# Kernel tuning notes

Measured on AMD Instinct MI355X. Metric: run time of the kernel, lower is better.

Reference implementation:

```python
import jax, jax.numpy as jnp
import numpy as np

C = 4096
N = 16384


def setup_inputs() -> dict:
    key = jax.random.key(0)
    k1, k2, k3 = jax.random.split(key, 3)
    x = jax.random.normal(k1, (N, C), dtype=jnp.float32)
    # fc params, torch default init: U(-1/sqrt(C), 1/sqrt(C))
    bound = 1.0 / np.sqrt(C)
    W = jax.random.uniform(k2, (C, C), dtype=jnp.float32, minval=-bound, maxval=bound)
    b = jax.random.uniform(k3, (C,), dtype=jnp.float32, minval=-bound, maxval=bound)
    return {"x": x, "W": W, "b": b, "scale_factor": 2}


def reference(x, W, b, scale_factor):
    # MyGAP_fc: mean over batch -> [1, C] (kept as [C])
    x_gap = jnp.mean(x, axis=0)                      # [C]
    # fc: torch Linear y = x @ W.T + b
    x_scale = x_gap @ W.T + b                        # [C]
    x_scale = jax.nn.sigmoid(x_scale * scale_factor) # [C]
    # training-mode path (no hard thresholding)
    # MyScale_fc: per-channel broadcast multiply
    x_out = x * x_scale[None, :]                     # [N, C]
    return (x_out, x_scale)
```

## Files before the change

kernel.cpp:

```cpp
#include <hip/hip_runtime.h>

#define C 4096
#define NROWS 16384
#define NBLK 256
#define TPB 1024
#define RPB 64
#define HWREG_XCC_ID 63508

typedef float f32x4 __attribute__((ext_vector_type(4)));

__device__ __forceinline__ unsigned aload(unsigned* p) {
    return __hip_atomic_load(p, __ATOMIC_RELAXED, __HIP_MEMORY_SCOPE_AGENT);
}
__device__ __forceinline__ unsigned aadd(unsigned* p, unsigned v) {
    return __hip_atomic_fetch_add(p, v, __ATOMIC_RELAXED, __HIP_MEMORY_SCOPE_AGENT);
}

#define CTRL_WORDS 2048

__device__ __forceinline__ void gbar(unsigned* ctrl, unsigned r, bool& lead,
                                     unsigned xcd) {
    __syncthreads();
    if (threadIdx.x == 0) {
        if (r == 1) {
            if (aadd(&ctrl[512 + 64 * xcd], 1u) == 0) {
                lead = true;
                unsigned lv = aadd(&ctrl[1088], 1u);
                asm volatile("" :: "v"(lv) : "memory");
            }
        }
        aadd(&ctrl[64 * xcd], 1u);
        if (lead) {
            for (;;) {
                unsigned s = 0;
#pragma unroll
                for (int i = 0; i < 8; ++i) s += aload(&ctrl[64 * i]);
                if (s >= r * NBLK) break;
                __builtin_amdgcn_s_sleep(2);
            }
            unsigned v = __hip_atomic_fetch_add(&ctrl[1024], 0u, __ATOMIC_ACQ_REL,
                                                __HIP_MEMORY_SCOPE_AGENT);
            asm volatile("" :: "v"(v) : "memory");
            aadd(&ctrl[1152], 1u);
            while (aload(&ctrl[1152]) < r * aload(&ctrl[1088]))
                __builtin_amdgcn_s_sleep(2);
            __hip_atomic_store(&ctrl[1280 + 64 * xcd], r, __ATOMIC_RELAXED,
                               __HIP_MEMORY_SCOPE_AGENT);
        } else {
            while (aload(&ctrl[1280 + 64 * xcd]) < r) __builtin_amdgcn_s_sleep(8);
        }
    }
    __syncthreads();
}

__global__ __launch_bounds__(TPB, 4)
void fused_kernel(const float* __restrict__ x, const float* __restrict__ W,
                  const float* __restrict__ b, const int* __restrict__ sf,
                  float* __restrict__ out, float* __restrict__ ws) {
    float* gsumX = ws;
    unsigned* ctrl = (unsigned*)(ws + 8 * (size_t)C);

    __shared__ float g_lds[C];

    const int t = threadIdx.x;
    const int bidx = blockIdx.x;
    const int r0 = bidx * RPB;
    const float sf0 = (float)sf[0];
    const unsigned xcd = __builtin_amdgcn_s_getreg(HWREG_XCC_ID) & 7u;
    bool lead = false;

    {
        const f32x4* xv = (const f32x4*)x + (size_t)r0 * (C / 4) + t;
        f32x4 acc = {0.f, 0.f, 0.f, 0.f};
#pragma unroll 8
        for (int r = 0; r < RPB; ++r)
            acc += xv[(size_t)r * (C / 4)];
        float* g = gsumX + (size_t)xcd * C + t * 4;
        atomicAdd(g + 0, acc.x);
        atomicAdd(g + 1, acc.y);
        atomicAdd(g + 2, acc.z);
        atomicAdd(g + 3, acc.w);
    }
    gbar(ctrl, 1, lead, xcd);

    {
        f32x4 s = {0.f, 0.f, 0.f, 0.f};
#pragma unroll
        for (int xx = 0; xx < 8; ++xx)
            s += ((const f32x4*)(gsumX + (size_t)xx * C))[t];
        ((f32x4*)g_lds)[t] = s;
    }
    __syncthreads();
    {
        const int wave = t >> 6, lane = t & 63;
        const int row = (bidx << 4) + wave;
        const f32x4* wv = (const f32x4*)(W + (size_t)row * C);
        const f32x4* gv = (const f32x4*)g_lds;
        float acc = 0.f;
#pragma unroll
        for (int i = 0; i < 16; ++i) {
            const f32x4 w4 = __builtin_nontemporal_load(wv + (i << 6) + lane);
            const f32x4 g4 = gv[(i << 6) + lane];
            acc += w4.x * g4.x + w4.y * g4.y + w4.z * g4.z + w4.w * g4.w;
        }
#pragma unroll
        for (int off = 32; off; off >>= 1) acc += __shfl_down(acc, off);
        if (lane == 0) {
            const float y = acc * (1.0f / NROWS) + b[row];
            out[(size_t)NROWS * C + row] = 1.0f / (1.0f + __expf(-sf0 * y));
        }
    }
    gbar(ctrl, 2, lead, xcd);

    {
        const f32x4 sc = ((const f32x4*)(out + (size_t)NROWS * C))[t];
        const f32x4* xv = (const f32x4*)x + (size_t)r0 * (C / 4) + t;
        f32x4* ov = (f32x4*)out + (size_t)r0 * (C / 4) + t;
#pragma unroll 8
        for (int r = 0; r < RPB; ++r) {
            f32x4 v = xv[(size_t)r * (C / 4)];
            v *= sc;
            __builtin_nontemporal_store(v, ov + (size_t)r * (C / 4));
        }
    }
}

extern "C" void kernel_launch(void* const* d_in, const int* in_sizes, int n_in,
                              void* d_out, int out_size, void* d_ws, size_t ws_size,
                              hipStream_t stream) {
    const float* x = (const float*)d_in[0];
    const float* W = (const float*)d_in[1];
    const float* b = (const float*)d_in[2];
    const int* sf  = (const int*)d_in[3];

    float* out = (float*)d_out;
    float* ws  = (float*)d_ws;

    hipMemsetAsync(d_ws, 0, (8 * (size_t)C) * sizeof(float)
                            + CTRL_WORDS * sizeof(unsigned), stream);

    fused_kernel<<<NBLK, TPB, 0, stream>>>(x, W, b, sf, out, ws);
}
```

Measured before the change: 180.7 us.

## Split column-sum into separate kernels and keep one grid barrier

```diff
diff --git a/kernel.cpp b/kernel.cpp
--- a/kernel.cpp
+++ b/kernel.cpp
@@ -2,10 +2,10 @@
 
 #define C 4096
 #define NROWS 16384
-#define NBLK 256
-#define TPB 1024
-#define RPB 64
+#define NBLK 512
 #define HWREG_XCC_ID 63508
+#define PARTS 256
+#define CTRL_WORDS 2048
 
 typedef float f32x4 __attribute__((ext_vector_type(4)));
 
@@ -16,18 +16,14 @@
     return __hip_atomic_fetch_add(p, v, __ATOMIC_RELAXED, __HIP_MEMORY_SCOPE_AGENT);
 }
 
-#define CTRL_WORDS 2048
-
-__device__ __forceinline__ void gbar(unsigned* ctrl, unsigned r, bool& lead,
-                                     unsigned xcd) {
+__device__ __forceinline__ void gbar(unsigned* ctrl, unsigned xcd) {
+    bool lead = false;
     __syncthreads();
     if (threadIdx.x == 0) {
-        if (r == 1) {
-            if (aadd(&ctrl[512 + 64 * xcd], 1u) == 0) {
-                lead = true;
-                unsigned lv = aadd(&ctrl[1088], 1u);
-                asm volatile("" :: "v"(lv) : "memory");
-            }
+        if (aadd(&ctrl[512 + 64 * xcd], 1u) == 0) {
+            lead = true;
+            unsigned lv = aadd(&ctrl[1088], 1u);
+            asm volatile("" :: "v"(lv) : "memory");
         }
         aadd(&ctrl[64 * xcd], 1u);
         if (lead) {
@@ -35,65 +31,62 @@
                 unsigned s = 0;
 #pragma unroll
                 for (int i = 0; i < 8; ++i) s += aload(&ctrl[64 * i]);
-                if (s >= r * NBLK) break;
+                if (s >= NBLK) break;
                 __builtin_amdgcn_s_sleep(2);
             }
             unsigned v = __hip_atomic_fetch_add(&ctrl[1024], 0u, __ATOMIC_ACQ_REL,
                                                 __HIP_MEMORY_SCOPE_AGENT);
             asm volatile("" :: "v"(v) : "memory");
             aadd(&ctrl[1152], 1u);
-            while (aload(&ctrl[1152]) < r * aload(&ctrl[1088]))
+            while (aload(&ctrl[1152]) < aload(&ctrl[1088]))
                 __builtin_amdgcn_s_sleep(2);
-            __hip_atomic_store(&ctrl[1280 + 64 * xcd], r, __ATOMIC_RELAXED,
+            __hip_atomic_store(&ctrl[1280 + 64 * xcd], 1u, __ATOMIC_RELAXED,
                                __HIP_MEMORY_SCOPE_AGENT);
         } else {
-            while (aload(&ctrl[1280 + 64 * xcd]) < r) __builtin_amdgcn_s_sleep(8);
+            while (aload(&ctrl[1280 + 64 * xcd]) < 1u) __builtin_amdgcn_s_sleep(8);
         }
     }
     __syncthreads();
 }
 
-__global__ __launch_bounds__(TPB, 4)
-void fused_kernel(const float* __restrict__ x, const float* __restrict__ W,
+__global__ void colsum_partial(const float* __restrict__ x, float* __restrict__ part) {
+    const int c4 = blockIdx.x * blockDim.x + threadIdx.x;
+    const int r0 = blockIdx.y * (NROWS / PARTS);
+    const f32x4* xv = (const f32x4*)x;
+    f32x4 acc = {0.f, 0.f, 0.f, 0.f};
+#pragma unroll 4
+    for (int r = 0; r < NROWS / PARTS; ++r)
+        acc += xv[(size_t)(r0 + r) * (C / 4) + c4];
+    __builtin_nontemporal_store(acc, (f32x4*)part + (size_t)blockIdx.y * (C / 4) + c4);
+}
+
+__global__ void colsum_reduce(const float* __restrict__ part, float* __restrict__ gsum) {
+    const int c = blockIdx.x * blockDim.x + threadIdx.x;
+    float s = 0.f;
+#pragma unroll 8
+    for (int r = 0; r < PARTS; ++r) s += part[(size_t)r * C + c];
+    gsum[c] = s;
+}
+
+__global__ __launch_bounds__(512, 8)
+void matvec_scale(const float* __restrict__ x, const float* __restrict__ W,
                   const float* __restrict__ b, const int* __restrict__ sf,
-                  float* __restrict__ out, float* __restrict__ ws) {
-    float* gsumX = ws;
-    unsigned* ctrl = (unsigned*)(ws + 8 * (size_t)C);
-
+                  const float* __restrict__ gsum, float* __restrict__ out,
+                  unsigned* __restrict__ ctrl) {
     __shared__ float g_lds[C];
 
     const int t = threadIdx.x;
     const int bidx = blockIdx.x;
-    const int r0 = bidx * RPB;
     const float sf0 = (float)sf[0];
     const unsigned xcd = __builtin_amdgcn_s_getreg(HWREG_XCC_ID) & 7u;
-    bool lead = false;
+
+    ((f32x4*)g_lds)[t]       = ((const f32x4*)gsum)[t];
+    ((f32x4*)g_lds)[t + 512] = ((const f32x4*)gsum)[t + 512];
+    __syncthreads();
 
     {
-        const f32x4* xv = (const f32x4*)x + (size_t)r0 * (C / 4) + t;
-        f32x4 acc = {0.f, 0.f, 0.f, 0.f};
-#pragma unroll 8
-        for (int r = 0; r < RPB; ++r)
-            acc += xv[(size_t)r * (C / 4)];
-        float* g = gsumX + (size_t)xcd * C + t * 4;
-        atomicAdd(g + 0, acc.x);
-        atomicAdd(g + 1, acc.y);
-        atomicAdd(g + 2, acc.z);
-        atomicAdd(g + 3, acc.w);
-    }
-    gbar(ctrl, 1, lead, xcd);
-
-    {
-        f32x4 s = {0.f, 0.f, 0.f, 0.f};
-#pragma unroll
-        for (int xx = 0; xx < 8; ++xx)
-            s += ((const f32x4*)(gsumX + (size_t)xx * C))[t];
-        ((f32x4*)g_lds)[t] = s;
-    }
-    __syncthreads();
-    {
         const int wave = t >> 6, lane = t & 63;
-        const int row = (bidx << 4) + wave;
+        const int row = (bidx << 3) + wave;
         const f32x4* wv = (const f32x4*)(W + (size_t)row * C);
         const f32x4* gv = (const f32x4*)g_lds;
         float acc = 0.f;
@@ -110,17 +103,23 @@
             out[(size_t)NROWS * C + row] = 1.0f / (1.0f + __expf(-sf0 * y));
         }
     }
-    gbar(ctrl, 2, lead, xcd);
+
+    gbar(ctrl, xcd);
 
     {
-        const f32x4 sc = ((const f32x4*)(out + (size_t)NROWS * C))[t];
-        const f32x4* xv = (const f32x4*)x + (size_t)r0 * (C / 4) + t;
-        f32x4* ov = (f32x4*)out + (size_t)r0 * (C / 4) + t;
-#pragma unroll 8
-        for (int r = 0; r < RPB; ++r) {
-            f32x4 v = xv[(size_t)r * (C / 4)];
-            v *= sc;
-            __builtin_nontemporal_store(v, ov + (size_t)r * (C / 4));
+        const f32x4* sv = (const f32x4*)(out + (size_t)NROWS * C);
+        const f32x4 sc0 = sv[t], sc1 = sv[t + 512];
+        const int r0 = bidx << 5;
+        const f32x4* xv = (const f32x4*)x + (size_t)r0 * (C / 4);
+        f32x4* ov = (f32x4*)out + (size_t)r0 * (C / 4);
+#pragma unroll 4
+        for (int r = 0; r < 32; ++r) {
+            f32x4 v0 = xv[(size_t)r * (C / 4) + t];
+            f32x4 v1 = xv[(size_t)r * (C / 4) + t + 512];
+            v0 *= sc0;
+            v1 *= sc1;
+            __builtin_nontemporal_store(v0, ov + (size_t)r * (C / 4) + t);
+            __builtin_nontemporal_store(v1, ov + (size_t)r * (C / 4) + t + 512);
         }
     }
 }
@@ -134,10 +133,13 @@
     const int* sf  = (const int*)d_in[3];
 
     float* out = (float*)d_out;
-    float* ws  = (float*)d_ws;
+    float* part = (float*)d_ws;
+    float* gsum = part + (size_t)PARTS * C;
+    unsigned* ctrl = (unsigned*)(gsum + C);
 
-    hipMemsetAsync(d_ws, 0, (8 * (size_t)C) * sizeof(float)
-                            + CTRL_WORDS * sizeof(unsigned), stream);
+    hipMemsetAsync(ctrl, 0, CTRL_WORDS * sizeof(unsigned), stream);
 
-    fused_kernel<<<NBLK, TPB, 0, stream>>>(x, W, b, sf, out, ws);
+    colsum_partial<<<dim3(4, PARTS), 256, 0, stream>>>(x, part);
+    colsum_reduce<<<C / 256, 256, 0, stream>>>(part, gsum);
+    matvec_scale<<<NBLK, 512, 0, stream>>>(x, W, b, sf, gsum, out, ctrl);
 }
```

Measured after the change: 165.6 us. 1.09x faster.
